# Kernel tuning notes

Hardware: AMD Instinct MI355X
Metric: run time of the kernel (lower is better)

## Reference

```python
import jax, jax.numpy as jnp
import numpy as np

# dims: batch, internal ticks, neurons, input dim, NLM memory length, NLM hidden, sync pairs, out dims
B, T_TICKS, D, D_IN, M, H, P, D_OUT, D_ACT = 512, 8, 2048, 512, 16, 4, 512, 512, 512


def setup_inputs() -> dict:
    key = jax.random.key(0)
    ks = jax.random.split(key, 16)
    n = lambda k, shape: jax.random.normal(k, shape, dtype=jnp.float32)
    return {
        "x": n(ks[0], (B, D_IN)),
        # input projection
        "W_in": n(ks[1], (D_IN, D)) * 0.02,
        "b_in": jnp.zeros((D,), jnp.float32),
        # learned start post-activation state
        "z0": n(ks[2], (D,)) * 0.02,
        # synapse model: concat(z, features) -> pre-activations
        "W_syn": n(ks[3], (D + D, D)) * 0.02,
        "b_syn": jnp.zeros((D,), jnp.float32),
        # privately parameterized neuron-level models (NeuronLevelModel)
        "nlm_w1": n(ks[4], (M, H, D)) * 0.02,
        "nlm_b1": jnp.zeros((1, H, D), jnp.float32),
        "nlm_w2": n(ks[5], (H, D)) * 0.02,
        "nlm_b2": jnp.zeros((1, D), jnp.float32),
        # neural synchronization (NeuralSynchronization)
        "decay_out": jnp.zeros((P,), jnp.float32),
        "decay_action": jnp.zeros((P,), jnp.float32),
        "W_out": n(ks[6], (P, D_OUT)) * 0.02,
        "b_out": jnp.zeros((D_OUT,), jnp.float32),
        "W_act": n(ks[7], (P, D_ACT)) * 0.02,
        "b_act": jnp.zeros((D_ACT,), jnp.float32),
        # random neuron index pairs (buffers, int)
        "pairs_out": jax.random.randint(ks[8], (P, 2), 0, D),
        "pairs_action": jax.random.randint(ks[9], (P, 2), 0, D),
    }


def _nlm(hist, w1, b1, w2, b2):
    # hist: (B, D, M); private per-neuron 2-layer MLP
    h = jnp.einsum('bdM,Mhd->bdh', hist, w1) + jnp.swapaxes(b1, 1, 2)  # (B, D, H)
    h = jax.nn.relu(h)
    return jnp.einsum('bdh,hd->bd', h, w2) + b2  # (B, D)


def reference(x, W_in, b_in, z0, W_syn, b_syn, nlm_w1, nlm_b1, nlm_w2, nlm_b2,
              decay_out, decay_action, W_out, b_out, W_act, b_act,
              pairs_out, pairs_action):
    feats = x @ W_in + b_in                      # (B, D)
    z = jnp.broadcast_to(z0, (x.shape[0], D))    # (B, D)
    hist = jnp.zeros((x.shape[0], D, M), x.dtype)
    # exponential-decay sync recurrence: S_t = exp(-|r|) * S_{t-1} + z_i z_j
    # equals sum_s z_{i,s} z_{j,s} exp(-|r| (t - s))  (matches compute_sync weights)
    r_out = jnp.exp(-jnp.abs(decay_out))         # (P,)
    r_act = jnp.exp(-jnp.abs(decay_action))
    S_out = jnp.zeros((x.shape[0], P), x.dtype)
    S_act = jnp.zeros((x.shape[0], P), x.dtype)
    ys, qs = [], []
    for _ in range(T_TICKS):
        pre = jnp.concatenate([z, feats], axis=-1) @ W_syn + b_syn     # (B, D)
        hist = jnp.concatenate([hist[..., 1:], pre[..., None]], axis=-1)
        z = _nlm(hist, nlm_w1, nlm_b1, nlm_w2, nlm_b2)                 # (B, D)
        S_out = S_out * r_out + z[:, pairs_out[:, 0]] * z[:, pairs_out[:, 1]]
        S_act = S_act * r_act + z[:, pairs_action[:, 0]] * z[:, pairs_action[:, 1]]
        ys.append(S_out @ W_out + b_out)
        qs.append(S_act @ W_act + b_act)
    return jnp.stack(ys, axis=1), jnp.stack(qs, axis=1)  # (B, T, d_out), (B, T, d_action)
```

## Files before the change

kernel.cpp:

```cpp
#include <hip/hip_runtime.h>
#include <math.h>

#define Bsz 512
#define TT 8
#define Dn 2048
#define DIN 512
#define Hh 4
#define Pn 512
#define DOUT 512
#define BD (Bsz*Dn)

typedef __attribute__((ext_vector_type(8))) short s16x8;
typedef __attribute__((ext_vector_type(4))) float f32x4;
typedef __attribute__((ext_vector_type(4))) unsigned short u16x4;

__device__ __forceinline__ unsigned short f2bf(float f) {
  unsigned int u = __float_as_uint(f);
  unsigned int r = (u + 0x7fffu + ((u >> 16) & 1u)) >> 16;
  return (unsigned short)r;
}
__device__ __forceinline__ float bf2f(unsigned short h) {
  return __uint_as_float(((unsigned int)h) << 16);
}
__device__ __forceinline__ void split2(float x, unsigned short& h, unsigned short& l) {
  h = f2bf(x);
  float r = x - bf2f(h);
  l = f2bf(r);
}

#define GLOAD16(g, l) __builtin_amdgcn_global_load_lds( \
    (const __attribute__((address_space(1))) unsigned int*)(g), \
    (__attribute__((address_space(3))) unsigned int*)(l), 16, 0, 0)

__device__ __forceinline__ void gemm_core(
    const unsigned short* __restrict__ Ah, const unsigned short* __restrict__ Al,
    const unsigned short* __restrict__ BTh, const unsigned short* __restrict__ BTl,
    int K, long arow0, long brow0,
    unsigned short* LDS, f32x4 acc[2][2], int g, int qw)
{
  const int tid = threadIdx.x;
  const int lane = tid & 63;
  const int lh = lane >> 4, sc = lane & 15;
  const unsigned short* gsrc[8];
  int ldst[8];
#pragma unroll
  for (int t = 0; t < 4; ++t) {
    int rb = qw * 16 + t * 4;
    int row = rb + lh;
    int ko = ((sc & 7) ^ (row & 7)) << 3;
    gsrc[t]     = (sc >= 8 ? Al : Ah) + (size_t)(arow0 + row) * K + ko;
    ldst[t]     = rb * 128;
    gsrc[4 + t] = (sc >= 8 ? BTl : BTh) + (size_t)(brow0 + row) * K + ko;
    ldst[4 + t] = 32768 + rb * 128;
  }

  const int nI = K >> 7;

#define STAGE(ring, i_)                                              \
  {                                                                  \
    const size_t kb = ((size_t)(2 * (i_) + g)) << 6;                 \
    unsigned short* base_ = LDS + (g * 2 + (ring)) * 8192;           \
    GLOAD16(gsrc[0] + kb, base_ + ldst[0]);                          \
    GLOAD16(gsrc[1] + kb, base_ + ldst[1]);                          \
    GLOAD16(gsrc[2] + kb, base_ + ldst[2]);                          \
    GLOAD16(gsrc[3] + kb, base_ + ldst[3]);                          \
    GLOAD16(gsrc[4] + kb, base_ + ldst[4]);                          \
    GLOAD16(gsrc[5] + kb, base_ + ldst[5]);                          \
    GLOAD16(gsrc[6] + kb, base_ + ldst[6]);                          \
    GLOAD16(gsrc[7] + kb, base_ + ldst[7]);                          \
  }

  const int wm = (qw & 1) * 32, wn = (qw >> 1) * 32;
  const int lm = lane & 15, kg4 = lane >> 4;
  int aoh[2][2], boh[2][2];
#pragma unroll
  for (int u = 0; u < 2; ++u) {
    int kg = u * 4 + kg4;
#pragma unroll
    for (int mt = 0; mt < 2; ++mt) {
      int ar = wm + mt * 16 + lm;
      aoh[u][mt] = ar * 128 + ((kg ^ (ar & 7)) << 3);
    }
#pragma unroll
    for (int nt = 0; nt < 2; ++nt) {
      int br = wn + nt * 16 + lm;
      boh[u][nt] = br * 128 + ((kg ^ (br & 7)) << 3);
    }
  }

  STAGE(0, 0);
  for (int i = 0; i < nI; ++i) {
    asm volatile("s_waitcnt vmcnt(0)" ::: "memory");
    __builtin_amdgcn_s_barrier();
    if (i + 1 < nI) STAGE((i + 1) & 1, i + 1);
    const unsigned short* ab = LDS + (g * 2 + (i & 1)) * 8192;
    const unsigned short* bb = ab + 32768;
#pragma unroll
    for (int u = 0; u < 2; ++u) {
      s16x8 fah[2], fal[2], fbh[2], fbl[2];
#pragma unroll
      for (int mt = 0; mt < 2; ++mt) {
        fah[mt] = *(const s16x8*)(ab + aoh[u][mt]);
        fal[mt] = *(const s16x8*)(ab + aoh[u][mt] + 64);
      }
#pragma unroll
      for (int nt = 0; nt < 2; ++nt) {
        fbh[nt] = *(const s16x8*)(bb + boh[u][nt]);
        fbl[nt] = *(const s16x8*)(bb + boh[u][nt] + 64);
      }
      __builtin_amdgcn_s_setprio(1);
#pragma unroll
      for (int mt = 0; mt < 2; ++mt)
#pragma unroll
        for (int nt = 0; nt < 2; ++nt) {
          acc[mt][nt] = __builtin_amdgcn_mfma_f32_16x16x32_bf16(fah[mt], fbh[nt], acc[mt][nt], 0, 0, 0);
          acc[mt][nt] = __builtin_amdgcn_mfma_f32_16x16x32_bf16(fah[mt], fbl[nt], acc[mt][nt], 0, 0, 0);
          acc[mt][nt] = __builtin_amdgcn_mfma_f32_16x16x32_bf16(fal[mt], fbh[nt], acc[mt][nt], 0, 0, 0);
        }
      __builtin_amdgcn_s_setprio(0);
    }
  }
#undef STAGE

  __builtin_amdgcn_s_barrier();
  float* fred = (float*)LDS;
  const int ridx = (qw * 64 + lane) * 17;
  if (g == 1) {
#pragma unroll
    for (int mt = 0; mt < 2; ++mt)
#pragma unroll
      for (int nt = 0; nt < 2; ++nt)
#pragma unroll
        for (int r = 0; r < 4; ++r)
          fred[ridx + (mt * 2 + nt) * 4 + r] = acc[mt][nt][r];
  }
  __builtin_amdgcn_s_barrier();
  if (g == 0) {
#pragma unroll
    for (int mt = 0; mt < 2; ++mt)
#pragma unroll
      for (int nt = 0; nt < 2; ++nt)
#pragma unroll
        for (int r = 0; r < 4; ++r)
          acc[mt][nt][r] += fred[ridx + (mt * 2 + nt) * 4 + r];
  }
}

template<int MODE>
__global__ __launch_bounds__(512, 1)
void mfma_gemm(const unsigned short* __restrict__ Ah, const unsigned short* __restrict__ Al,
               const unsigned short* __restrict__ BTh, const unsigned short* __restrict__ BTl,
               const float* __restrict__ bias, float* __restrict__ Cf,
               unsigned short* __restrict__ Ch, unsigned short* __restrict__ Cl,
               int M, int N, int K, int gm, int gn)
{
  __shared__ unsigned short LDS[65536];
  int bid = blockIdx.x;
  int xcd = bid & 7, w = bid >> 3;
  int bmi = w % gm, bni = xcd * (gn >> 3) + w / gm;
  long bm = (long)bmi * 64, bn = (long)bni * 64;
  const int tid = threadIdx.x, lane = tid & 63, wave = tid >> 6;
  const int g = wave >> 2, qw = wave & 3;
  f32x4 acc[2][2];
#pragma unroll
  for (int a = 0; a < 2; ++a)
#pragma unroll
    for (int b = 0; b < 2; ++b) acc[a][b] = (f32x4)0.f;
  gemm_core(Ah, Al, BTh, BTl, K, bm, bn, LDS, acc, g, qw);
  if (g == 1) return;

  const int wm = (qw & 1) * 32, wn = (qw >> 1) * 32;
#pragma unroll
  for (int nt = 0; nt < 2; ++nt) {
    int n = (int)bn + wn + nt * 16 + (lane & 15);
    float bv = bias[n];
#pragma unroll
    for (int mt = 0; mt < 2; ++mt) {
      long r0 = bm + wm + mt * 16 + (lane >> 4) * 4;
#pragma unroll
      for (int r = 0; r < 4; ++r) {
        float v = acc[mt][nt][r] + bv;
        long R = r0 + r;
        if (MODE == 0) {
          unsigned short h_, l_; split2(v, h_, l_);
          Ch[R * N + n] = h_; Cl[R * N + n] = l_;
        } else {
          Cf[R * N + n] = v;
        }
      }
    }
  }
}

__global__ __launch_bounds__(512, 1)
void out_gemm(const unsigned short* __restrict__ S0h, const unsigned short* __restrict__ S0l,
              const unsigned short* __restrict__ S1h, const unsigned short* __restrict__ S1l,
              const unsigned short* __restrict__ W0h, const unsigned short* __restrict__ W0l,
              const unsigned short* __restrict__ W1h, const unsigned short* __restrict__ W1l,
              const float* __restrict__ bias0, const float* __restrict__ bias1,
              float* __restrict__ out0, float* __restrict__ out1)
{
  __shared__ unsigned short LDS[65536];
  const int set = blockIdx.y;
  const unsigned short* Ah = set ? S1h : S0h;
  const unsigned short* Al = set ? S1l : S0l;
  const unsigned short* BTh = set ? W1h : W0h;
  const unsigned short* BTl = set ? W1l : W0l;
  const float* bias = set ? bias1 : bias0;
  float* Cf = set ? out1 : out0;

  int bid = blockIdx.x;
  int xcd = bid & 7, w = bid >> 3;
  int bmi = w % 64, bni = xcd + (w / 64) * 8;
  long bm = (long)bmi * 64, bn = (long)bni * 64;
  const int tid = threadIdx.x, lane = tid & 63, wave = tid >> 6;
  const int g = wave >> 2, qw = wave & 3;
  f32x4 acc[2][2];
#pragma unroll
  for (int a = 0; a < 2; ++a)
#pragma unroll
    for (int b = 0; b < 2; ++b) acc[a][b] = (f32x4)0.f;
  gemm_core(Ah, Al, BTh, BTl, Pn, bm, bn, LDS, acc, g, qw);
  if (g == 1) return;

  const int wm = (qw & 1) * 32, wn = (qw >> 1) * 32;
#pragma unroll
  for (int nt = 0; nt < 2; ++nt) {
    int n = (int)bn + wn + nt * 16 + (lane & 15);
    float bv = bias[n];
#pragma unroll
    for (int mt = 0; mt < 2; ++mt) {
      long r0 = bm + wm + mt * 16 + (lane >> 4) * 4;
#pragma unroll
      for (int r = 0; r < 4; ++r) {
        float v = acc[mt][nt][r] + bv;
        long R = r0 + r;
        long t = R >> 9, b = R & 511;
        Cf[(b * TT + t) * DOUT + n] = v;
      }
    }
  }
}

template<int TAU>
__global__ __launch_bounds__(512, 1)
void tick_mfma(const unsigned short* __restrict__ zh, const unsigned short* __restrict__ zl,
               const unsigned short* __restrict__ WTh, const unsigned short* __restrict__ WTl,
               const float* __restrict__ basep, const float* __restrict__ hist,
               float* __restrict__ histout,
               const float* __restrict__ w1, const float* __restrict__ b1,
               const float* __restrict__ w2, const float* __restrict__ b2,
               unsigned short* __restrict__ zho, unsigned short* __restrict__ zlo,
               unsigned short* __restrict__ zT)
{
  __shared__ unsigned short LDS[65536];
  int bid = blockIdx.x;
  int xcd = bid & 7, w = bid >> 3;
  int bmi = w % 8, bni = xcd * 4 + w / 8;
  long bm = (long)bmi * 64, bn = (long)bni * 64;
  const int tid = threadIdx.x, lane = tid & 63, wave = tid >> 6;
  const int g = wave >> 2, qw = wave & 3;
  f32x4 acc[2][2];
#pragma unroll
  for (int a = 0; a < 2; ++a)
#pragma unroll
    for (int b = 0; b < 2; ++b) acc[a][b] = (f32x4)0.f;
  gemm_core(zh, zl, WTh, WTl, Dn, bm, bn, LDS, acc, g, qw);
  if (g == 1) return;

  const int wm = (qw & 1) * 32, wn = (qw >> 1) * 32;
#pragma unroll
  for (int nt = 0; nt < 2; ++nt) {
    const int d = (int)bn + wn + nt * 16 + (lane & 15);
    float w2v[Hh], b1v[Hh];
#pragma unroll
    for (int hh = 0; hh < Hh; ++hh) {
      w2v[hh] = w2[hh * Dn + d];
      b1v[hh] = b1[hh * Dn + d];
    }
    const float b2v = b2[d];
#pragma unroll
    for (int mt = 0; mt < 2; ++mt) {
      const int b0 = (int)bm + wm + mt * 16 + (lane >> 4) * 4;
      float pre[4], hacc[4][Hh];
#pragma unroll
      for (int r = 0; r < 4; ++r) {
        pre[r] = acc[mt][nt][r] + basep[(size_t)(b0 + r) * Dn + d];
#pragma unroll
        for (int hh = 0; hh < Hh; ++hh) hacc[r][hh] = b1v[hh];
      }
#pragma unroll
      for (int s = 0; s < TAU; ++s) {
        float wv[Hh];
#pragma unroll
        for (int hh = 0; hh < Hh; ++hh) wv[hh] = w1[((15 - TAU + s) * Hh + hh) * Dn + d];
#pragma unroll
        for (int r = 0; r < 4; ++r) {
          float psv = hist[(size_t)s * BD + (size_t)(b0 + r) * Dn + d];
#pragma unroll
          for (int hh = 0; hh < Hh; ++hh) hacc[r][hh] = fmaf(psv, wv[hh], hacc[r][hh]);
        }
      }
      {
        float wv[Hh];
#pragma unroll
        for (int hh = 0; hh < Hh; ++hh) wv[hh] = w1[(15 * Hh + hh) * Dn + d];
#pragma unroll
        for (int r = 0; r < 4; ++r)
#pragma unroll
          for (int hh = 0; hh < Hh; ++hh) hacc[r][hh] = fmaf(pre[r], wv[hh], hacc[r][hh]);
      }
      u16x4 pack;
#pragma unroll
      for (int r = 0; r < 4; ++r) {
        histout[(size_t)(b0 + r) * Dn + d] = pre[r];
        float z = b2v;
#pragma unroll
        for (int hh = 0; hh < Hh; ++hh) z = fmaf(fmaxf(hacc[r][hh], 0.f), w2v[hh], z);
        unsigned short h_, l_; split2(z, h_, l_);
        zho[(size_t)(b0 + r) * Dn + d] = h_;
        zlo[(size_t)(b0 + r) * Dn + d] = l_;
        pack[r] = f2bf(z);
      }
      *(u16x4*)&zT[(size_t)d * Bsz + b0] = pack;
    }
  }
}

__global__ __launch_bounds__(256)
void tick0_kernel(const float* __restrict__ basep, const float* __restrict__ qpart,
                  float* __restrict__ histout,
                  const float* __restrict__ w1, const float* __restrict__ b1,
                  const float* __restrict__ w2, const float* __restrict__ b2,
                  unsigned short* __restrict__ zho, unsigned short* __restrict__ zlo,
                  unsigned short* __restrict__ zT)
{
  int g = blockIdx.x * 256 + threadIdx.x;
  int b = g >> 8;
  int d0 = (g & 255) * 8;
  float qv[8];
#pragma unroll
  for (int k = 0; k < 8; ++k) qv[k] = 0.f;
#pragma unroll
  for (int c = 0; c < 8; ++c) {
    float4 p0 = *(const float4*)(qpart + (size_t)c * Dn + d0);
    float4 p1 = *(const float4*)(qpart + (size_t)c * Dn + d0 + 4);
    qv[0] += p0.x; qv[1] += p0.y; qv[2] += p0.z; qv[3] += p0.w;
    qv[4] += p1.x; qv[5] += p1.y; qv[6] += p1.z; qv[7] += p1.w;
  }
#pragma unroll
  for (int k = 0; k < 8; ++k) {
    int d = d0 + k;
    float pre = basep[(size_t)b * Dn + d] + qv[k];
    histout[(size_t)b * Dn + d] = pre;
    float z = b2[d];
#pragma unroll
    for (int hh = 0; hh < Hh; ++hh) {
      float h = fmaf(pre, w1[(15 * Hh + hh) * Dn + d], b1[hh * Dn + d]);
      z = fmaf(fmaxf(h, 0.f), w2[hh * Dn + d], z);
    }
    unsigned short h_, l_; split2(z, h_, l_);
    zho[(size_t)b * Dn + d] = h_;
    zlo[(size_t)b * Dn + d] = l_;
    zT[(size_t)d * Bsz + b] = f2bf(z);
  }
}

__global__ __launch_bounds__(512)
void sync_kernel(const unsigned short* __restrict__ zT,
                 const int* __restrict__ pairs0, const int* __restrict__ pairs1,
                 const float* __restrict__ decay0, const float* __restrict__ decay1,
                 unsigned short* __restrict__ Sh0, unsigned short* __restrict__ Sl0,
                 unsigned short* __restrict__ Sh1, unsigned short* __restrict__ Sl1)
{
  __shared__ float Ls[8][8][65];
  const int set = blockIdx.y;
  const int* pairs = set ? pairs1 : pairs0;
  const float* decay = set ? decay1 : decay0;
  unsigned short* Sh = set ? Sh1 : Sh0;
  unsigned short* Sl = set ? Sl1 : Sl0;
  const int tid = threadIdx.x;
  const int lb = tid & 63, pl = tid >> 6;
  const int p = blockIdx.x * 8 + pl;
  const int i = pairs[2 * p], j = pairs[2 * p + 1];
  const float r = expf(-fabsf(decay[p]));
  const int pb = tid & 7, bb2 = tid >> 3;
  for (int bb = 0; bb < 8; ++bb) {
    int b = bb * 64 + lb;
    float S = 0.f, St[8];
#pragma unroll
    for (int t = 0; t < 8; ++t) {
      float zi = bf2f(zT[(size_t)t * BD + (size_t)i * Bsz + b]);
      float zj = bf2f(zT[(size_t)t * BD + (size_t)j * Bsz + b]);
      S = fmaf(S, r, zi * zj);
      St[t] = S;
    }
#pragma unroll
    for (int t = 0; t < 8; ++t) Ls[pl][t][lb] = St[t];
    __syncthreads();
#pragma unroll
    for (int t = 0; t < 8; ++t) {
      float v = Ls[pb][t][bb2];
      unsigned short h_, l_; split2(v, h_, l_);
      size_t off = ((size_t)t * Bsz + bb * 64 + bb2) * Pn + blockIdx.x * 8 + pb;
      Sh[off] = h_; Sl[off] = l_;
    }
    __syncthreads();
  }
}

__device__ __forceinline__ void transpose_tile(const float* __restrict__ in, int ldin,
    unsigned short* __restrict__ Th, unsigned short* __restrict__ Tl, int K,
    int kb, int nb, float T[64][65])
{
  int k0 = kb * 64, n0 = nb * 64;
  int tid = threadIdx.x;
  int r = tid >> 2, c0 = (tid & 3) * 16;
#pragma unroll
  for (int cc = 0; cc < 16; cc += 4) {
    float4 v = *(const float4*)(in + (size_t)(k0 + r) * ldin + n0 + c0 + cc);
    T[c0 + cc + 0][r] = v.x; T[c0 + cc + 1][r] = v.y;
    T[c0 + cc + 2][r] = v.z; T[c0 + cc + 3][r] = v.w;
  }
  __syncthreads();
  int n = tid >> 2, kc = (tid & 3) * 16;
#pragma unroll
  for (int kk = 0; kk < 16; ++kk) {
    float v = T[n][kc + kk];
    unsigned short h_, l_; split2(v, h_, l_);
    Th[(size_t)(n0 + n) * K + k0 + kc + kk] = h_;
    Tl[(size_t)(n0 + n) * K + k0 + kc + kk] = l_;
  }
}

__global__ __launch_bounds__(256)
void prep_kernel(const float* __restrict__ W_syn, const float* __restrict__ W_in,
                 const float* __restrict__ W_out, const float* __restrict__ W_act,
                 const float* __restrict__ x, const float* __restrict__ z0,
                 unsigned short* WtTh, unsigned short* WtTl,
                 unsigned short* WbTh, unsigned short* WbTl,
                 unsigned short* WinTh, unsigned short* WinTl,
                 unsigned short* WoTh, unsigned short* WoTl,
                 unsigned short* WaTh, unsigned short* WaTl,
                 unsigned short* xh, unsigned short* xl,
                 float* qpart)
{
  __shared__ float T[64][65];
  const int b = blockIdx.x;
  const int tid = threadIdx.x;
  if (b < 1024) {
    transpose_tile(W_syn, Dn, WtTh, WtTl, Dn, b & 31, b >> 5, T);
  } else if (b < 2048) {
    int b2 = b - 1024;
    transpose_tile(W_syn + (size_t)Dn * Dn, Dn, WbTh, WbTl, Dn, b2 & 31, b2 >> 5, T);
  } else if (b < 2304) {
    int b2 = b - 2048;
    transpose_tile(W_in, Dn, WinTh, WinTl, DIN, b2 & 7, b2 >> 3, T);
  } else if (b < 2368) {
    int b2 = b - 2304;
    transpose_tile(W_out, DOUT, WoTh, WoTl, Pn, b2 & 7, b2 >> 3, T);
  } else if (b < 2432) {
    int b2 = b - 2368;
    transpose_tile(W_act, DOUT, WaTh, WaTl, Pn, b2 & 7, b2 >> 3, T);
  } else if (b < 2688) {
    int i = (b - 2432) * 256 + tid;
    float4 v = *(const float4*)(x + (size_t)i * 4);
    u16x4 h, l;
    unsigned short th, tl;
    split2(v.x, th, tl); h[0] = th; l[0] = tl;
    split2(v.y, th, tl); h[1] = th; l[1] = tl;
    split2(v.z, th, tl); h[2] = th; l[2] = tl;
    split2(v.w, th, tl); h[3] = th; l[3] = tl;
    *(u16x4*)(xh + (size_t)i * 4) = h;
    *(u16x4*)(xl + (size_t)i * 4) = l;
  } else {
    int idx = b - 2688;
    int colb = idx & 31, kc = idx >> 5;
    float (*red)[64] = (float(*)[64])T;
    const int c = tid & 63, strip = tid >> 6;
    const int col = colb * 64 + c;
    const int k0 = (kc * 4 + strip) * 64;
    float acc = 0.f;
#pragma unroll 8
    for (int k = k0; k < k0 + 64; ++k)
      acc = fmaf(z0[k], W_syn[(size_t)k * Dn + col], acc);
    red[strip][c] = acc;
    __syncthreads();
    if (strip == 0)
      qpart[(size_t)kc * Dn + col] = red[0][c] + red[1][c] + red[2][c] + red[3][c];
  }
}

extern "C" void kernel_launch(void* const* d_in, const int* in_sizes, int n_in,
                              void* d_out, int out_size, void* d_ws, size_t ws_size,
                              hipStream_t stream) {
  const float* x      = (const float*)d_in[0];
  const float* W_in   = (const float*)d_in[1];
  const float* b_in   = (const float*)d_in[2];
  const float* z0     = (const float*)d_in[3];
  const float* W_syn  = (const float*)d_in[4];
  const float* b_syn  = (const float*)d_in[5];
  const float* w1     = (const float*)d_in[6];
  const float* b1     = (const float*)d_in[7];
  const float* w2     = (const float*)d_in[8];
  const float* b2     = (const float*)d_in[9];
  const float* decay_out = (const float*)d_in[10];
  const float* decay_act = (const float*)d_in[11];
  const float* W_out  = (const float*)d_in[12];
  const float* b_out  = (const float*)d_in[13];
  const float* W_act  = (const float*)d_in[14];
  const float* b_act  = (const float*)d_in[15];
  const int* pairs_out = (const int*)d_in[16];
  const int* pairs_act = (const int*)d_in[17];

  char* W = (char*)d_ws;
  auto alloc = [&](size_t bytes) { char* p = W; W += (bytes + 255) & ~255ull; return p; };
  unsigned short* WtTh = (unsigned short*)alloc((size_t)Dn * Dn * 2);
  unsigned short* WtTl = (unsigned short*)alloc((size_t)Dn * Dn * 2);
  unsigned short* WbTh = (unsigned short*)alloc((size_t)Dn * Dn * 2);
  unsigned short* WbTl = (unsigned short*)alloc((size_t)Dn * Dn * 2);
  unsigned short* WinTh = (unsigned short*)alloc((size_t)Dn * DIN * 2);
  unsigned short* WinTl = (unsigned short*)alloc((size_t)Dn * DIN * 2);
  unsigned short* WoTh = (unsigned short*)alloc((size_t)DOUT * Pn * 2);
  unsigned short* WoTl = (unsigned short*)alloc((size_t)DOUT * Pn * 2);
  unsigned short* WaTh = (unsigned short*)alloc((size_t)DOUT * Pn * 2);
  unsigned short* WaTl = (unsigned short*)alloc((size_t)DOUT * Pn * 2);
  unsigned short* xh = (unsigned short*)alloc((size_t)Bsz * DIN * 2);
  unsigned short* xl = (unsigned short*)alloc((size_t)Bsz * DIN * 2);
  unsigned short* fh = (unsigned short*)alloc((size_t)BD * 2);
  unsigned short* fl = (unsigned short*)alloc((size_t)BD * 2);
  float* qpart = (float*)alloc(8 * Dn * 4);
  float* base  = (float*)alloc((size_t)BD * 4);
  float* hist  = (float*)alloc((size_t)TT * BD * 4);
  unsigned short* zbh[2], *zbl[2];
  zbh[0] = (unsigned short*)alloc((size_t)BD * 2);
  zbl[0] = (unsigned short*)alloc((size_t)BD * 2);
  zbh[1] = (unsigned short*)alloc((size_t)BD * 2);
  zbl[1] = (unsigned short*)alloc((size_t)BD * 2);
  unsigned short* zT = (unsigned short*)alloc((size_t)TT * BD * 2);
  unsigned short* Sh0 = WbTh;
  unsigned short* Sl0 = WbTh + (size_t)TT * Bsz * Pn;
  unsigned short* Sh1 = WbTl;
  unsigned short* Sl1 = WbTl + (size_t)TT * Bsz * Pn;

  float* outy = (float*)d_out;
  float* outq = outy + (size_t)Bsz * TT * DOUT;

  dim3 blk(256);
  dim3 blk512(512);
  prep_kernel<<<dim3(2944), blk, 0, stream>>>(
      W_syn, W_in, W_out, W_act, x, z0,
      WtTh, WtTl, WbTh, WbTl, WinTh, WinTl, WoTh, WoTl, WaTh, WaTl,
      xh, xl, qpart);
  mfma_gemm<0><<<dim3(256), blk512, 0, stream>>>(xh, xl, WinTh, WinTl, b_in, nullptr, fh, fl,
                                                 Bsz, Dn, DIN, 8, 32);
  mfma_gemm<1><<<dim3(256), blk512, 0, stream>>>(fh, fl, WbTh, WbTl, b_syn, base, nullptr, nullptr,
                                                 Bsz, Dn, Dn, 8, 32);
  tick0_kernel<<<dim3(512), blk, 0, stream>>>(base, qpart, hist, w1, b1, w2, b2,
                                              zbh[0], zbl[0], zT);
  for (int tau = 1; tau < TT; ++tau) {
    const unsigned short* zih = zbh[(tau + 1) & 1];
    const unsigned short* zil = zbl[(tau + 1) & 1];
    unsigned short* zoh = zbh[tau & 1];
    unsigned short* zol = zbl[tau & 1];
    float* ho = hist + (size_t)tau * BD;
    unsigned short* zTo = zT + (size_t)tau * BD;
    switch (tau) {
      case 1: tick_mfma<1><<<dim3(256), blk512, 0, stream>>>(zih, zil, WtTh, WtTl, base, hist, ho, w1, b1, w2, b2, zoh, zol, zTo); break;
      case 2: tick_mfma<2><<<dim3(256), blk512, 0, stream>>>(zih, zil, WtTh, WtTl, base, hist, ho, w1, b1, w2, b2, zoh, zol, zTo); break;
      case 3: tick_mfma<3><<<dim3(256), blk512, 0, stream>>>(zih, zil, WtTh, WtTl, base, hist, ho, w1, b1, w2, b2, zoh, zol, zTo); break;
      case 4: tick_mfma<4><<<dim3(256), blk512, 0, stream>>>(zih, zil, WtTh, WtTl, base, hist, ho, w1, b1, w2, b2, zoh, zol, zTo); break;
      case 5: tick_mfma<5><<<dim3(256), blk512, 0, stream>>>(zih, zil, WtTh, WtTl, base, hist, ho, w1, b1, w2, b2, zoh, zol, zTo); break;
      case 6: tick_mfma<6><<<dim3(256), blk512, 0, stream>>>(zih, zil, WtTh, WtTl, base, hist, ho, w1, b1, w2, b2, zoh, zol, zTo); break;
      case 7: tick_mfma<7><<<dim3(256), blk512, 0, stream>>>(zih, zil, WtTh, WtTl, base, hist, ho, w1, b1, w2, b2, zoh, zol, zTo); break;
    }
  }
  sync_kernel<<<dim3(Pn / 8, 2), dim3(512), 0, stream>>>(zT, pairs_out, pairs_act,
                                                         decay_out, decay_act,
                                                         Sh0, Sl0, Sh1, Sl1);
  out_gemm<<<dim3(512, 2), blk512, 0, stream>>>(Sh0, Sl0, Sh1, Sl1,
                                                WoTh, WoTl, WaTh, WaTl,
                                                b_out, b_act, outy, outq);
}
```

Measured before the change: 285.6 us.

## Split split-K reduction across both wave groups and fuse tick0 into base GEMM

The cross-group reduction in the GEMM core is now symmetric: each wave group writes the half of its accumulators owned by the other group and adds the partner's partial sums for its own half. The epilogue work is therefore split between both groups instead of idling group 1. The base GEMM and the tick-0 neuron model are fused into one kernel, which saves a launch and a reread of the base pre-activations. The trade-off is more per-thread epilogue state in the fused kernel, with less coalesced indexing than the old elementwise tick0 kernel.

```diff
diff --git a/kernel.cpp b/kernel.cpp
--- a/kernel.cpp
+++ b/kernel.cpp
@@ -124,26 +124,20 @@
 
   __builtin_amdgcn_s_barrier();
   float* fred = (float*)LDS;
-  const int ridx = (qw * 64 + lane) * 17;
-  if (g == 1) {
-#pragma unroll
-    for (int mt = 0; mt < 2; ++mt)
-#pragma unroll
-      for (int nt = 0; nt < 2; ++nt)
-#pragma unroll
-        for (int r = 0; r < 4; ++r)
-          fred[ridx + (mt * 2 + nt) * 4 + r] = acc[mt][nt][r];
-  }
+  const int oth = 1 - g;
+  const int widx = ((g * 4 + qw) * 64 + lane) * 9;
+#pragma unroll
+  for (int mt = 0; mt < 2; ++mt)
+#pragma unroll
+    for (int r = 0; r < 4; ++r)
+      fred[widx + mt * 4 + r] = acc[mt][oth][r];
   __builtin_amdgcn_s_barrier();
-  if (g == 0) {
-#pragma unroll
-    for (int mt = 0; mt < 2; ++mt)
-#pragma unroll
-      for (int nt = 0; nt < 2; ++nt)
-#pragma unroll
-        for (int r = 0; r < 4; ++r)
-          acc[mt][nt][r] += fred[ridx + (mt * 2 + nt) * 4 + r];
-  }
+  const int pidx = ((oth * 4 + qw) * 64 + lane) * 9;
+#pragma unroll
+  for (int mt = 0; mt < 2; ++mt)
+#pragma unroll
+    for (int r = 0; r < 4; ++r)
+      acc[mt][g][r] += fred[pidx + mt * 4 + r];
 }
 
 template<int MODE>
@@ -167,26 +161,23 @@
 #pragma unroll
     for (int b = 0; b < 2; ++b) acc[a][b] = (f32x4)0.f;
   gemm_core(Ah, Al, BTh, BTl, K, bm, bn, LDS, acc, g, qw);
-  if (g == 1) return;
 
   const int wm = (qw & 1) * 32, wn = (qw >> 1) * 32;
-#pragma unroll
-  for (int nt = 0; nt < 2; ++nt) {
-    int n = (int)bn + wn + nt * 16 + (lane & 15);
-    float bv = bias[n];
-#pragma unroll
-    for (int mt = 0; mt < 2; ++mt) {
-      long r0 = bm + wm + mt * 16 + (lane >> 4) * 4;
-#pragma unroll
-      for (int r = 0; r < 4; ++r) {
-        float v = acc[mt][nt][r] + bv;
-        long R = r0 + r;
-        if (MODE == 0) {
-          unsigned short h_, l_; split2(v, h_, l_);
-          Ch[R * N + n] = h_; Cl[R * N + n] = l_;
-        } else {
-          Cf[R * N + n] = v;
-        }
+  const int nt = g;
+  int n = (int)bn + wn + nt * 16 + (lane & 15);
+  float bv = bias[n];
+#pragma unroll
+  for (int mt = 0; mt < 2; ++mt) {
+    long r0 = bm + wm + mt * 16 + (lane >> 4) * 4;
+#pragma unroll
+    for (int r = 0; r < 4; ++r) {
+      float v = acc[mt][nt][r] + bv;
+      long R = r0 + r;
+      if (MODE == 0) {
+        unsigned short h_, l_; split2(v, h_, l_);
+        Ch[R * N + n] = h_; Cl[R * N + n] = l_;
+      } else {
+        Cf[R * N + n] = v;
       }
     }
   }
@@ -221,23 +212,20 @@
 #pragma unroll
     for (int b = 0; b < 2; ++b) acc[a][b] = (f32x4)0.f;
   gemm_core(Ah, Al, BTh, BTl, Pn, bm, bn, LDS, acc, g, qw);
-  if (g == 1) return;
 
   const int wm = (qw & 1) * 32, wn = (qw >> 1) * 32;
-#pragma unroll
-  for (int nt = 0; nt < 2; ++nt) {
-    int n = (int)bn + wn + nt * 16 + (lane & 15);
-    float bv = bias[n];
-#pragma unroll
-    for (int mt = 0; mt < 2; ++mt) {
-      long r0 = bm + wm + mt * 16 + (lane >> 4) * 4;
-#pragma unroll
-      for (int r = 0; r < 4; ++r) {
-        float v = acc[mt][nt][r] + bv;
-        long R = r0 + r;
-        long t = R >> 9, b = R & 511;
-        Cf[(b * TT + t) * DOUT + n] = v;
-      }
+  const int nt = g;
+  int n = (int)bn + wn + nt * 16 + (lane & 15);
+  float bv = bias[n];
+#pragma unroll
+  for (int mt = 0; mt < 2; ++mt) {
+    long r0 = bm + wm + mt * 16 + (lane >> 4) * 4;
+#pragma unroll
+    for (int r = 0; r < 4; ++r) {
+      float v = acc[mt][nt][r] + bv;
+      long R = r0 + r;
+      long t = R >> 9, b = R & 511;
+      Cf[(b * TT + t) * DOUT + n] = v;
     }
   }
 }
@@ -266,103 +254,126 @@
 #pragma unroll
     for (int b = 0; b < 2; ++b) acc[a][b] = (f32x4)0.f;
   gemm_core(zh, zl, WTh, WTl, Dn, bm, bn, LDS, acc, g, qw);
-  if (g == 1) return;
 
   const int wm = (qw & 1) * 32, wn = (qw >> 1) * 32;
-#pragma unroll
-  for (int nt = 0; nt < 2; ++nt) {
-    const int d = (int)bn + wn + nt * 16 + (lane & 15);
-    float w2v[Hh], b1v[Hh];
-#pragma unroll
-    for (int hh = 0; hh < Hh; ++hh) {
-      w2v[hh] = w2[hh * Dn + d];
-      b1v[hh] = b1[hh * Dn + d];
-    }
-    const float b2v = b2[d];
-#pragma unroll
-    for (int mt = 0; mt < 2; ++mt) {
-      const int b0 = (int)bm + wm + mt * 16 + (lane >> 4) * 4;
-      float pre[4], hacc[4][Hh];
+  const int nt = g;
+  const int d = (int)bn + wn + nt * 16 + (lane & 15);
+  float w2v[Hh], b1v[Hh];
+#pragma unroll
+  for (int hh = 0; hh < Hh; ++hh) {
+    w2v[hh] = w2[hh * Dn + d];
+    b1v[hh] = b1[hh * Dn + d];
+  }
+  const float b2v = b2[d];
+#pragma unroll
+  for (int mt = 0; mt < 2; ++mt) {
+    const int b0 = (int)bm + wm + mt * 16 + (lane >> 4) * 4;
+    float pre[4], hacc[4][Hh];
+#pragma unroll
+    for (int r = 0; r < 4; ++r) {
+      pre[r] = acc[mt][nt][r] + basep[(size_t)(b0 + r) * Dn + d];
+#pragma unroll
+      for (int hh = 0; hh < Hh; ++hh) hacc[r][hh] = b1v[hh];
+    }
+#pragma unroll
+    for (int s = 0; s < TAU; ++s) {
+      float wv[Hh];
+#pragma unroll
+      for (int hh = 0; hh < Hh; ++hh) wv[hh] = w1[((15 - TAU + s) * Hh + hh) * Dn + d];
 #pragma unroll
       for (int r = 0; r < 4; ++r) {
-        pre[r] = acc[mt][nt][r] + basep[(size_t)(b0 + r) * Dn + d];
-#pragma unroll
-        for (int hh = 0; hh < Hh; ++hh) hacc[r][hh] = b1v[hh];
+        float psv = hist[(size_t)s * BD + (size_t)(b0 + r) * Dn + d];
+#pragma unroll
+        for (int hh = 0; hh < Hh; ++hh) hacc[r][hh] = fmaf(psv, wv[hh], hacc[r][hh]);
       }
-#pragma unroll
-      for (int s = 0; s < TAU; ++s) {
-        float wv[Hh];
-#pragma unroll
-        for (int hh = 0; hh < Hh; ++hh) wv[hh] = w1[((15 - TAU + s) * Hh + hh) * Dn + d];
-#pragma unroll
-        for (int r = 0; r < 4; ++r) {
-          float psv = hist[(size_t)s * BD + (size_t)(b0 + r) * Dn + d];
-#pragma unroll
-          for (int hh = 0; hh < Hh; ++hh) hacc[r][hh] = fmaf(psv, wv[hh], hacc[r][hh]);
-        }
+    }
+    {
+      float wv[Hh];
+#pragma unroll
+      for (int hh = 0; hh < Hh; ++hh) wv[hh] = w1[(15 * Hh + hh) * Dn + d];
+#pragma unroll
+      for (int r = 0; r < 4; ++r)
+#pragma unroll
+        for (int hh = 0; hh < Hh; ++hh) hacc[r][hh] = fmaf(pre[r], wv[hh], hacc[r][hh]);
+    }
+    u16x4 pack;
+#pragma unroll
+    for (int r = 0; r < 4; ++r) {
+      histout[(size_t)(b0 + r) * Dn + d] = pre[r];
+      float z = b2v;
+#pragma unroll
+      for (int hh = 0; hh < Hh; ++hh) z = fmaf(fmaxf(hacc[r][hh], 0.f), w2v[hh], z);
+      unsigned short h_, l_; split2(z, h_, l_);
+      zho[(size_t)(b0 + r) * Dn + d] = h_;
+      zlo[(size_t)(b0 + r) * Dn + d] = l_;
+      pack[r] = f2bf(z);
+    }
+    *(u16x4*)&zT[(size_t)d * Bsz + b0] = pack;
+  }
+}
+
+__global__ __launch_bounds__(512, 1)
+void base_tick0(const unsigned short* __restrict__ fh, const unsigned short* __restrict__ fl,
+                const unsigned short* __restrict__ WbTh, const unsigned short* __restrict__ WbTl,
+                const float* __restrict__ b_syn, float* __restrict__ basep,
+                const float* __restrict__ qpart,
+                const float* __restrict__ w1, const float* __restrict__ b1,
+                const float* __restrict__ w2, const float* __restrict__ b2,
+                float* __restrict__ hist0,
+                unsigned short* __restrict__ zho, unsigned short* __restrict__ zlo,
+                unsigned short* __restrict__ zT)
+{
+  __shared__ unsigned short LDS[65536];
+  int bid = blockIdx.x;
+  int xcd = bid & 7, w = bid >> 3;
+  int bmi = w % 8, bni = xcd * 4 + w / 8;
+  long bm = (long)bmi * 64, bn = (long)bni * 64;
+  const int tid = threadIdx.x, lane = tid & 63, wave = tid >> 6;
+  const int g = wave >> 2, qw = wave & 3;
+  f32x4 acc[2][2];
+#pragma unroll
+  for (int a = 0; a < 2; ++a)
+#pragma unroll
+    for (int b = 0; b < 2; ++b) acc[a][b] = (f32x4)0.f;
+  gemm_core(fh, fl, WbTh, WbTl, Dn, bm, bn, LDS, acc, g, qw);
+
+  const int wm = (qw & 1) * 32, wn = (qw >> 1) * 32;
+  const int nt = g;
+  const int d = (int)bn + wn + nt * 16 + (lane & 15);
+  const float bv = b_syn[d];
+  float qv = 0.f;
+#pragma unroll
+  for (int c = 0; c < 8; ++c) qv += qpart[(size_t)c * Dn + d];
+  float w1v[Hh], b1v[Hh], w2v[Hh];
+#pragma unroll
+  for (int hh = 0; hh < Hh; ++hh) {
+    w1v[hh] = w1[(15 * Hh + hh) * Dn + d];
+    b1v[hh] = b1[hh * Dn + d];
+    w2v[hh] = w2[hh * Dn + d];
+  }
+  const float b2v = b2[d];
+#pragma unroll
+  for (int mt = 0; mt < 2; ++mt) {
+    const int b0 = (int)bm + wm + mt * 16 + (lane >> 4) * 4;
+    u16x4 pack;
+#pragma unroll
+    for (int r = 0; r < 4; ++r) {
+      float v = acc[mt][nt][r] + bv;
+      basep[(size_t)(b0 + r) * Dn + d] = v;
+      float pre = v + qv;
+      hist0[(size_t)(b0 + r) * Dn + d] = pre;
+      float z = b2v;
+#pragma unroll
+      for (int hh = 0; hh < Hh; ++hh) {
+        float h = fmaf(pre, w1v[hh], b1v[hh]);
+        z = fmaf(fmaxf(h, 0.f), w2v[hh], z);
       }
-      {
-        float wv[Hh];
-#pragma unroll
-        for (int hh = 0; hh < Hh; ++hh) wv[hh] = w1[(15 * Hh + hh) * Dn + d];
-#pragma unroll
-        for (int r = 0; r < 4; ++r)
-#pragma unroll
-          for (int hh = 0; hh < Hh; ++hh) hacc[r][hh] = fmaf(pre[r], wv[hh], hacc[r][hh]);
-      }
-      u16x4 pack;
-#pragma unroll
-      for (int r = 0; r < 4; ++r) {
-        histout[(size_t)(b0 + r) * Dn + d] = pre[r];
-        float z = b2v;
-#pragma unroll
-        for (int hh = 0; hh < Hh; ++hh) z = fmaf(fmaxf(hacc[r][hh], 0.f), w2v[hh], z);
-        unsigned short h_, l_; split2(z, h_, l_);
-        zho[(size_t)(b0 + r) * Dn + d] = h_;
-        zlo[(size_t)(b0 + r) * Dn + d] = l_;
-        pack[r] = f2bf(z);
-      }
-      *(u16x4*)&zT[(size_t)d * Bsz + b0] = pack;
-    }
-  }
-}
-
-__global__ __launch_bounds__(256)
-void tick0_kernel(const float* __restrict__ basep, const float* __restrict__ qpart,
-                  float* __restrict__ histout,
-                  const float* __restrict__ w1, const float* __restrict__ b1,
-                  const float* __restrict__ w2, const float* __restrict__ b2,
-                  unsigned short* __restrict__ zho, unsigned short* __restrict__ zlo,
-                  unsigned short* __restrict__ zT)
-{
-  int g = blockIdx.x * 256 + threadIdx.x;
-  int b = g >> 8;
-  int d0 = (g & 255) * 8;
-  float qv[8];
-#pragma unroll
-  for (int k = 0; k < 8; ++k) qv[k] = 0.f;
-#pragma unroll
-  for (int c = 0; c < 8; ++c) {
-    float4 p0 = *(const float4*)(qpart + (size_t)c * Dn + d0);
-    float4 p1 = *(const float4*)(qpart + (size_t)c * Dn + d0 + 4);
-    qv[0] += p0.x; qv[1] += p0.y; qv[2] += p0.z; qv[3] += p0.w;
-    qv[4] += p1.x; qv[5] += p1.y; qv[6] += p1.z; qv[7] += p1.w;
-  }
-#pragma unroll
-  for (int k = 0; k < 8; ++k) {
-    int d = d0 + k;
-    float pre = basep[(size_t)b * Dn + d] + qv[k];
-    histout[(size_t)b * Dn + d] = pre;
-    float z = b2[d];
-#pragma unroll
-    for (int hh = 0; hh < Hh; ++hh) {
-      float h = fmaf(pre, w1[(15 * Hh + hh) * Dn + d], b1[hh * Dn + d]);
-      z = fmaf(fmaxf(h, 0.f), w2[hh * Dn + d], z);
-    }
-    unsigned short h_, l_; split2(z, h_, l_);
-    zho[(size_t)b * Dn + d] = h_;
-    zlo[(size_t)b * Dn + d] = l_;
-    zT[(size_t)d * Bsz + b] = f2bf(z);
+      unsigned short h_, l_; split2(z, h_, l_);
+      zho[(size_t)(b0 + r) * Dn + d] = h_;
+      zlo[(size_t)(b0 + r) * Dn + d] = l_;
+      pack[r] = f2bf(z);
+    }
+    *(u16x4*)&zT[(size_t)d * Bsz + b0] = pack;
   }
 }
 
@@ -554,10 +565,9 @@
       xh, xl, qpart);
   mfma_gemm<0><<<dim3(256), blk512, 0, stream>>>(xh, xl, WinTh, WinTl, b_in, nullptr, fh, fl,
                                                  Bsz, Dn, DIN, 8, 32);
-  mfma_gemm<1><<<dim3(256), blk512, 0, stream>>>(fh, fl, WbTh, WbTl, b_syn, base, nullptr, nullptr,
-                                                 Bsz, Dn, Dn, 8, 32);
-  tick0_kernel<<<dim3(512), blk, 0, stream>>>(base, qpart, hist, w1, b1, w2, b2,
-                                              zbh[0], zbl[0], zT);
+  base_tick0<<<dim3(256), blk512, 0, stream>>>(fh, fl, WbTh, WbTl, b_syn, base, qpart,
+                                               w1, b1, w2, b2, hist,
+                                               zbh[0], zbl[0], zT);
   for (int tau = 1; tau < TT; ++tau) {
     const unsigned short* zih = zbh[(tau + 1) & 1];
     const unsigned short* zil = zbl[(tau + 1) & 1];
```

After: 313.5 us. +9.8%, slower.
